# Optimization experiments

Hardware: AMD Instinct MI355X
Metric: run time of the kernel (lower is better)

The kernel has to match this reference:

```python
import jax, jax.numpy as jnp
import numpy as np

ENC_DIM = 512
B, T = 2048, 256
NUM_PARTS, PART_DIM, ATT_DIM, VOCAB = 64, 32, 128, 12


def _p(key, shape, scale=0.05):
    return jax.random.normal(key, shape, dtype=jnp.float32) * scale


def setup_inputs() -> dict:
    key = jax.random.key(0)
    ks = jax.random.split(key, 24)
    inp = {
        "img_features": jax.random.normal(ks[0], (B, 32, 8, 8), dtype=jnp.float32),
        "label": jax.random.normal(ks[1], (B, T, VOCAB), dtype=jnp.float32),
        # Attention params
        "Ww": _p(ks[2], (ATT_DIM, PART_DIM)), "Wb": _p(ks[3], (ATT_DIM,)),
        "Uw": _p(ks[4], (ATT_DIM, ENC_DIM)), "Ub": _p(ks[5], (ATT_DIM,)),
        "vw": _p(ks[6], (1, ATT_DIM)), "vb": _p(ks[7], (1,)),
        "betaw": _p(ks[8], (PART_DIM, ENC_DIM)), "betab": _p(ks[9], (PART_DIM,)),
        # init hidden params
        "ihw": _p(ks[10], (ENC_DIM, NUM_PARTS)), "ihb": _p(ks[11], (ENC_DIM,)),
        "icw": _p(ks[12], (ENC_DIM, NUM_PARTS)), "icb": _p(ks[13], (ENC_DIM,)),
        # LSTMCell params (PyTorch layout: [4*H, in] / [4*H, H])
        "W_ih": _p(ks[14], (4 * ENC_DIM, VOCAB + PART_DIM)),
        "W_hh": _p(ks[15], (4 * ENC_DIM, ENC_DIM)),
        "b_ih": _p(ks[16], (4 * ENC_DIM,)), "b_hh": _p(ks[17], (4 * ENC_DIM,)),
        # output fc
        "ow": _p(ks[18], (VOCAB, ENC_DIM)), "ob": _p(ks[19], (VOCAB,)),
    }
    return inp


def reference(img_features, label, Ww, Wb, Uw, Ub, vw, vb, betaw, betab,
              ihw, ihb, icw, icb, W_ih, W_hh, b_ih, b_hh, ow, ob):
    b = img_features.shape[0]
    feats = img_features.reshape(b, 32, -1)          # [B, 32, 64]
    parts = feats.transpose(0, 2, 1)                  # [B, 64, 32]
    # init hidden/cell from mean over channel dim (dim=1 in torch)
    avg = feats.mean(axis=1)                          # [B, 64]
    h0 = jnp.tanh(avg @ ihw.T + ihb)                  # [B, H]
    c0 = jnp.tanh(avg @ icw.T + icb)
    # W_s depends only on img features: hoist out of the loop (same math)
    Ws = parts @ Ww.T + Wb                            # [B, 64, 128]
    lab = label.transpose(1, 0, 2)                    # [T, B, 12]

    H = h0.shape[1]

    def step(carry, x_t):
        h, c = carry
        Uh = h @ Uw.T + Ub                            # [B, 128]
        att = jnp.tanh(Ws + Uh[:, None, :])           # [B, 64, 128]
        score = (att @ vw.T + vb)[..., 0]             # [B, 64]
        alpha = jax.nn.softmax(score, axis=1)
        ctx = jnp.einsum('bp,bpd->bd', alpha, parts)  # [B, 32]
        beta = jax.nn.sigmoid(h @ betaw.T + betab)
        ctx = ctx * beta
        inp = jnp.concatenate([x_t, ctx], axis=1)     # [B, 44]
        gates = inp @ W_ih.T + b_ih + h @ W_hh.T + b_hh
        i, f, g, o = jnp.split(gates, 4, axis=1)
        c2 = jax.nn.sigmoid(f) * c + jax.nn.sigmoid(i) * jnp.tanh(g)
        h2 = jax.nn.sigmoid(o) * jnp.tanh(c2)
        out = h2 @ ow.T + ob                          # [B, 12]
        return (h2, c2), (out, alpha)

    (_, _), (outs, alphas) = jax.lax.scan(step, (h0, c0), lab)
    output = jax.nn.log_softmax(outs, axis=-1).transpose(1, 0, 2)  # [B, T, 12]
    return output, alphas  # alphas: [T, B, 64] (stacked version of the list)
```

## Files before the change

### kernel.cpp

```cpp
#include <hip/hip_runtime.h>
#include <hip/hip_bf16.h>


typedef __attribute__((ext_vector_type(8))) short short8;
typedef __attribute__((ext_vector_type(4))) float floatx4;
typedef __attribute__((ext_vector_type(2))) unsigned int uint2v;

#define DEV static __device__ __forceinline__
#define C2LE 2.885390082f
#define LOG2E 1.4426950409f
#define LN2 0.6931471806f

DEV unsigned short f2bf(float f) {
    unsigned int u = __float_as_uint(f);
    unsigned int r = (u + 0x7FFFu + ((u >> 16) & 1u)) >> 16;
    return (unsigned short)r;
}
DEV float bf2f(unsigned short u) { return __uint_as_float(((unsigned int)u) << 16); }
DEV float rcp_f(float x) { float r; asm("v_rcp_f32 %0, %1" : "=v"(r) : "v"(x)); return r; }
DEV float tanh_f(float x) { return 1.f - 2.f * rcp_f(1.f + exp2f(x * C2LE)); }
DEV float sigm(float x) { return rcp_f(1.f + exp2f(-x * LOG2E)); }

DEV void ldg16_sc(short8* d, const unsigned short* p) {
    asm volatile("global_load_dwordx4 %0, %1, off sc0 sc1" : "=v"(*d) : "v"(p));
}
DEV void stg16_sc(unsigned short* p, short8 v) {
    asm volatile("global_store_dwordx4 %0, %1, off sc0 sc1" :: "v"(p), "v"(v) : "memory");
}
DEV void stg8_sc(unsigned short* p, uint2v v) {
    asm volatile("global_store_dwordx2 %0, %1, off sc0 sc1" :: "v"(p), "v"(v) : "memory");
}
DEV void st_flag(int* p, int v) {
    asm volatile("global_store_dword %0, %1, off sc0 sc1" :: "v"(p), "v"(v) : "memory");
}
DEV int ld_flag(const int* p) {
    int v;
    asm volatile("global_load_dword %0, %1, off sc0 sc1\n\ts_waitcnt vmcnt(0)"
                 : "=v"(v) : "v"(p) : "memory");
    return v;
}
DEV void waitv0() { asm volatile("s_waitcnt vmcnt(0)" ::: "memory"); }

#define OFF_XH     ((size_t)0)
#define OFF_C0     ((size_t)2359296)
#define OFF_PARTS  ((size_t)6553600)
#define OFF_WBIG   ((size_t)14942208)
#define OFF_WSMALL ((size_t)17301504)
#define OFF_WW2    ((size_t)17465344)
#define OFF_BIAS   ((size_t)17473536)
#define OFF_AVG    ((size_t)17481728)
#define OFF_FLAGS  ((size_t)18006016)

DEV void gbar(int* flags, int bk, int g4, int step) {
    waitv0();
    __syncthreads();
    if (threadIdx.x < 64) {
        int lane = threadIdx.x;
        if (lane == 0) st_flag(flags + bk * 32, step);
        for (;;) {
            int v = step;
            if (lane < 4) v = ld_flag(flags + (g4 + lane) * 32);
            if (__all(v >= step)) break;
            __builtin_amdgcn_s_sleep(1);
        }
    }
    __syncthreads();
}

__global__ void k_init(int* flags) {
    int i = blockIdx.x * 256 + threadIdx.x;
    if (i < 256 * 32) flags[i] = 0;
}

__global__ void k_avg(const float* __restrict__ img, float* __restrict__ avg) {
    int idx = blockIdx.x * 256 + threadIdx.x;
    int b = idx >> 6, p = idx & 63;
    const float* base = img + (size_t)b * 2048 + p;
    float s = 0.f;
#pragma unroll
    for (int k = 0; k < 32; ++k) s += base[k * 64];
    avg[idx] = s * (1.f / 32.f);
}

__global__ void k_prep(const float* __restrict__ Whh, const float* __restrict__ Wih,
                       const float* __restrict__ Uw, const float* __restrict__ betaw,
                       const float* __restrict__ Ww, const float* __restrict__ bih,
                       const float* __restrict__ bhh,
                       unsigned short* __restrict__ Wbig, unsigned short* __restrict__ Wsmall,
                       unsigned short* __restrict__ Ww2, float* __restrict__ bias_cat) {
    int p = blockIdx.x, tid = threadIdx.x;
    int g = p & 3, j = p >> 2, orig = g * 512 + j;
    for (int k = tid; k < 576; k += 256) {
        float v = 0.f;
        if (k < 512) v = Whh[(size_t)orig * 512 + k];
        else if (k < 556) v = Wih[(size_t)orig * 44 + (k - 512)];
        Wbig[(size_t)p * 576 + k] = f2bf(v);
    }
    if (p < 160) {
        for (int k = tid; k < 512; k += 256) {
            float v = (p < 128) ? Uw[(size_t)p * 512 + k] : betaw[(size_t)(p - 128) * 512 + k];
            Wsmall[(size_t)p * 512 + k] = f2bf(v);
        }
    }
    if (p < 128 && tid < 32) Ww2[p * 32 + tid] = f2bf(C2LE * Ww[p * 32 + tid]);
    if (tid == 0) bias_cat[orig] = bih[orig] + bhh[orig];
}

__global__ __launch_bounds__(512) void k_h0c0(const float* __restrict__ avg,
                                              const float* __restrict__ ihw, const float* __restrict__ ihb,
                                              const float* __restrict__ icw, const float* __restrict__ icb,
                                              unsigned short* __restrict__ xh, float* __restrict__ c0) {
    __shared__ float avg_s[8][64];
    int b0 = blockIdx.x * 8, tid = threadIdx.x;
    for (int i = tid; i < 8 * 64; i += 512) avg_s[i >> 6][i & 63] = avg[b0 * 64 + i];
    __syncthreads();
    int j = tid;
    float w0[64];
#pragma unroll
    for (int p4 = 0; p4 < 16; ++p4) {
        float4 v = ((const float4*)(ihw + j * 64))[p4];
        w0[p4 * 4 + 0] = v.x; w0[p4 * 4 + 1] = v.y; w0[p4 * 4 + 2] = v.z; w0[p4 * 4 + 3] = v.w;
    }
    float bh = ihb[j];
#pragma unroll
    for (int bb = 0; bb < 8; ++bb) {
        float s = bh;
#pragma unroll
        for (int p = 0; p < 64; ++p) s += w0[p] * avg_s[bb][p];
        xh[(size_t)(b0 + bb) * 576 + j] = f2bf(tanh_f(s));
        if (j < 20) xh[(size_t)(b0 + bb) * 576 + 556 + j] = 0;
    }
#pragma unroll
    for (int p4 = 0; p4 < 16; ++p4) {
        float4 v = ((const float4*)(icw + j * 64))[p4];
        w0[p4 * 4 + 0] = v.x; w0[p4 * 4 + 1] = v.y; w0[p4 * 4 + 2] = v.z; w0[p4 * 4 + 3] = v.w;
    }
    float bc = icb[j];
#pragma unroll
    for (int bb = 0; bb < 8; ++bb) {
        float s = bc;
#pragma unroll
        for (int p = 0; p < 64; ++p) s += w0[p] * avg_s[bb][p];
        c0[(size_t)(b0 + bb) * 512 + j] = tanh_f(s);
    }
}

__global__ __launch_bounds__(256) void k_parts(const float* __restrict__ img,
                                               unsigned short* __restrict__ parts_bf) {
    __shared__ float pl[64][33];
    int b = blockIdx.x, tid = threadIdx.x;
    const float* ib = img + (size_t)b * 2048;
    for (int i = tid; i < 2048; i += 256) pl[i & 63][i >> 6] = ib[i];
    __syncthreads();
    for (int i = tid; i < 2048; i += 256)
        parts_bf[(size_t)b * 2048 + i] = f2bf(pl[i >> 5][i & 31]);
}

__global__ __launch_bounds__(512, 2) void k_scan(
    unsigned short* __restrict__ xh,
    const float* __restrict__ c0,
    const unsigned short* __restrict__ parts_bf,
    const unsigned short* __restrict__ Wsmall, const unsigned short* __restrict__ Wbig,
    const unsigned short* __restrict__ Ww2, const float* __restrict__ bias_cat,
    const float* __restrict__ Ub, const float* __restrict__ betab, const float* __restrict__ Wb,
    const float* __restrict__ vw,
    const float* __restrict__ label, const float* __restrict__ ow, const float* __restrict__ ob,
    float* __restrict__ out_alpha, float* __restrict__ out_logits,
    int* __restrict__ flags)
{
    __shared__ unsigned short Ald[32 * 584];
    __shared__ unsigned short parts_l[8][2304];
    __shared__ unsigned short ow_l[12][512];
    __shared__ unsigned short h2scr[32][128];
    __shared__ float uh_l[8][160];
    __shared__ float al_l[8][64];
    __shared__ float bias_l[512];
    __shared__ unsigned short xscr[8][48];
    __shared__ float vw2_l[128];
    __shared__ float obl[12];

    const int tid = threadIdx.x, w = tid >> 6, lane = tid & 63;
    const int bk = blockIdx.x;
    const int mtile = bk >> 2, ntile = bk & 3;
    const int g4 = bk & ~3;
    const int wm = w >> 2, wn = w & 3;

    if (tid < 128) vw2_l[tid] = -2.f * vw[tid];
    if (tid < 12) obl[tid] = ob[tid];
    {
        int g = tid >> 7, jl = tid & 127;
        bias_l[tid] = bias_cat[g * 512 + ntile * 128 + jl];
    }
    for (int i = tid; i < 12 * 512; i += 512) ow_l[i >> 9][i & 511] = f2bf(ow[i]);
    {
        int row = tid >> 6, p = tid & 63;
        const short8* src = (const short8*)(parts_bf + (size_t)(bk * 8 + row) * 2048 + p * 32);
        short8* dst = (short8*)&parts_l[row][p * 36];
        dst[0] = src[0]; dst[1] = src[1]; dst[2] = src[2]; dst[3] = src[3];
    }
    float creg[32];
#pragma unroll
    for (int nf = 0; nf < 8; ++nf)
#pragma unroll
        for (int r = 0; r < 4; ++r) {
            int b = mtile * 32 + wm * 16 + (lane >> 4) * 4 + r;
            int j = ntile * 128 + wn * 32 + nf * 4 + (lane & 3);
            creg[nf * 4 + r] = c0[(size_t)b * 512 + j];
        }
    {
        short8 tv[4];
#pragma unroll
        for (int q = 0; q < 4; ++q) {
            int cid = tid + q * 512;
            int row = cid >> 6, c16 = cid & 63;
            ldg16_sc(&tv[q], xh + (size_t)(mtile * 32 + row) * 576 + c16 * 8);
        }
        waitv0();
        __builtin_amdgcn_sched_barrier(0);
#pragma unroll
        for (int q = 0; q < 4; ++q) {
            int cid = tid + q * 512;
            int row = cid >> 6, c16 = cid & 63;
            *(short8*)&Ald[row * 584 + c16 * 8] = tv[q];
        }
    }
    __syncthreads();
    float vwsum = 0.f;
#pragma unroll
    for (int d = 0; d < 128; ++d) vwsum += vw2_l[d];
    vwsum *= -0.5f;

    auto do_uh = [&]() {
        if (w < 5) {
            const unsigned short* Bp = Wsmall + (size_t)(w * 32 + (lane & 15)) * 512 + (lane >> 4) * 8;
            const unsigned short* Ab = &Ald[(ntile * 8 + (lane & 7)) * 584 + (lane >> 4) * 8];
            floatx4 u0 = {}, u1 = {};
#pragma unroll 4
            for (int k0 = 0; k0 < 512; k0 += 32) {
                short8 a = *(const short8*)(Ab + k0);
                u0 = __builtin_amdgcn_mfma_f32_16x16x32_bf16(a, *(const short8*)(Bp + k0), u0, 0, 0, 0);
                u1 = __builtin_amdgcn_mfma_f32_16x16x32_bf16(a, *(const short8*)(Bp + 16 * 512 + k0), u1, 0, 0, 0);
            }
            int r0 = (lane >> 4) * 4, cc = lane & 15;
            if (r0 < 8) {
#pragma unroll
                for (int q = 0; q < 2; ++q) {
                    int n = w * 32 + q * 16 + cc;
#pragma unroll
                    for (int r = 0; r < 4; ++r) {
                        float val = (q ? u1[r] : u0[r]);
                        uh_l[r0 + r][n] = (n < 128) ? C2LE * (val + Ub[n] + Wb[n])
                                                    : (val + betab[n - 128]);
                    }
                }
            }
        }
    };

    auto do_head = [&](int tt) {
        int b = bk * 8 + w;
        short8 hv = *(const short8*)&Ald[(ntile * 8 + w) * 584 + lane * 8];
        float hf[8];
#pragma unroll
        for (int j = 0; j < 8; ++j) hf[j] = bf2f((unsigned short)hv[j]);
        float ov[12];
#pragma unroll
        for (int v = 0; v < 12; ++v) {
            short8 wv = *(const short8*)&ow_l[v][lane * 8];
            float p = 0.f;
#pragma unroll
            for (int j = 0; j < 8; ++j) p += hf[j] * bf2f((unsigned short)wv[j]);
#pragma unroll
            for (int o = 32; o; o >>= 1) p += __shfl_xor(p, o);
            ov[v] = p + obl[v];
        }
        float mx = ov[0];
#pragma unroll
        for (int v = 1; v < 12; ++v) mx = fmaxf(mx, ov[v]);
        float ss = 0.f;
#pragma unroll
        for (int v = 0; v < 12; ++v) ss += exp2f((ov[v] - mx) * LOG2E);
        float lse = mx + log2f(ss) * LN2;
#pragma unroll
        for (int v = 0; v < 12; ++v)
            if (lane == v) out_logits[((size_t)b * 256 + tt) * 12 + v] = ov[v] - lse;
    };

    auto do_attn = [&](int tt) {
        int b = bk * 8 + w;
        short8 pa[4];
#pragma unroll
        for (int mt = 0; mt < 4; ++mt)
            pa[mt] = *(const short8*)&parts_l[w][(mt * 16 + (lane & 15)) * 36 + (lane >> 4) * 8];
        float sc[4][4] = {};
#pragma unroll
        for (int nt = 0; nt < 8; ++nt) {
            short8 wwf = *(const short8*)(Ww2 + (size_t)((lane & 15) + 16 * nt) * 32 + (lane >> 4) * 8);
            int d = nt * 16 + (lane & 15);
            float ud = uh_l[w][d];
            float v2 = vw2_l[d];
#pragma unroll
            for (int mt = 0; mt < 4; ++mt) {
                floatx4 z = {};
                floatx4 wsa = __builtin_amdgcn_mfma_f32_16x16x32_bf16(pa[mt], wwf, z, 0, 0, 0);
#pragma unroll
                for (int r = 0; r < 4; ++r)
                    sc[mt][r] += v2 * rcp_f(1.f + exp2f(wsa[r] + ud));
            }
        }
        float mx = -1e30f;
#pragma unroll
        for (int mt = 0; mt < 4; ++mt)
#pragma unroll
            for (int r = 0; r < 4; ++r) {
                float s = sc[mt][r];
                s += __shfl_xor(s, 1); s += __shfl_xor(s, 2);
                s += __shfl_xor(s, 4); s += __shfl_xor(s, 8);
                s += vwsum;
                sc[mt][r] = s;
                mx = fmaxf(mx, s);
            }
        mx = fmaxf(mx, __shfl_xor(mx, 16));
        mx = fmaxf(mx, __shfl_xor(mx, 32));
        float ssum = 0.f;
        float av[4][4];
#pragma unroll
        for (int mt = 0; mt < 4; ++mt)
#pragma unroll
            for (int r = 0; r < 4; ++r) {
                av[mt][r] = exp2f((sc[mt][r] - mx) * LOG2E);
                ssum += av[mt][r];
            }
        ssum += __shfl_xor(ssum, 16);
        ssum += __shfl_xor(ssum, 32);
        float rs = rcp_f(ssum);
#pragma unroll
        for (int mt = 0; mt < 4; ++mt) {
            if ((lane & 15) == mt) {
                float4 fv = make_float4(av[mt][0] * rs, av[mt][1] * rs, av[mt][2] * rs, av[mt][3] * rs);
                int p0 = mt * 16 + (lane >> 4) * 4;
                *(float4*)&out_alpha[((size_t)tt * 2048 + b) * 64 + p0] = fv;
                *(float4*)&al_l[w][p0] = fv;
            }
        }
        int k = lane & 31, half = lane >> 5;
        float cp = 0.f;
#pragma unroll
        for (int p = 0; p < 32; ++p) {
            int pp = half * 32 + p;
            cp += al_l[w][pp] * bf2f(parts_l[w][pp * 36 + k]);
        }
        cp += __shfl_xor(cp, 32);
        if (half == 0) xscr[w][12 + k] = f2bf(cp * sigm(uh_l[w][128 + k]));
        if (lane < 12) xscr[w][lane] = f2bf(label[((size_t)b * 256 + tt) * 12 + lane]);
        if (lane < 11) {
            uint2v v = *(const uint2v*)&xscr[w][lane * 4];
            stg8_sc(xh + (size_t)b * 576 + 512 + lane * 4, v);
        }
    };

    auto phase1 = [&]() {
        const unsigned short* Bp = Wbig + (size_t)(ntile * 512 + wn * 128 + (lane & 15)) * 576 + (lane >> 4) * 8;
        const unsigned short* Ab = &Ald[(wm * 16 + (lane & 15)) * 584 + (lane >> 4) * 8];
        floatx4 acc[8] = {};
#pragma unroll 2
        for (int kk = 0; kk < 18; ++kk) {
            int k0 = kk * 32;
            short8 a = *(const short8*)(Ab + k0);
#pragma unroll
            for (int nf = 0; nf < 8; ++nf) {
                short8 bv = *(const short8*)(Bp + (size_t)nf * 9216 + k0);
                acc[nf] = __builtin_amdgcn_mfma_f32_16x16x32_bf16(a, bv, acc[nf], 0, 0, 0);
            }
        }
        int base = (lane & 48) | ((lane & 3) * 4);
#pragma unroll
        for (int nf = 0; nf < 8; ++nf) {
            int jl = wn * 32 + nf * 4 + (lane & 3);
            float bi = bias_l[jl], bfv = bias_l[128 + jl], bg = bias_l[256 + jl], bo = bias_l[384 + jl];
#pragma unroll
            for (int r = 0; r < 4; ++r) {
                float x = acc[nf][r];
                float g0 = __shfl(x, base + 0);
                float g1 = __shfl(x, base + 1);
                float g2 = __shfl(x, base + 2);
                float g3 = __shfl(x, base + 3);
                int ci = nf * 4 + r;
                float c2 = sigm(g1 + bfv) * creg[ci] + sigm(g0 + bi) * tanh_f(g2 + bg);
                creg[ci] = c2;
                float h2 = sigm(g3 + bo) * tanh_f(c2);
                if (((lane >> 2) & 3) == 0) {
                    int row = wm * 16 + (lane >> 4) * 4 + r;
                    h2scr[row][wn * 32 + nf * 4 + (lane & 3)] = f2bf(h2);
                }
            }
        }
        __syncthreads();
        {
            int row = tid >> 4, seg = tid & 15;
            short8 v = *(const short8*)&h2scr[row][seg * 8];
            stg16_sc(xh + (size_t)(mtile * 32 + row) * 576 + ntile * 128 + seg * 8, v);
        }
    };

    do_uh();
    __syncthreads();
    do_attn(0);
    int bc = 0;
    gbar(flags, bk, g4, ++bc);
    if (tid < 256) {
        short8 tv;
        int row = tid >> 3, c16 = tid & 7;
        ldg16_sc(&tv, xh + (size_t)(mtile * 32 + row) * 576 + 512 + c16 * 8);
        waitv0();
        __builtin_amdgcn_sched_barrier(0);
        *(short8*)&Ald[row * 584 + 512 + c16 * 8] = tv;
    }
    __syncthreads();

    for (int t = 0; t < 256; ++t) {
        phase1();
        gbar(flags, bk, g4, ++bc);
        {
            short8 tv;
            int row = tid >> 6, c16 = tid & 63;
            ldg16_sc(&tv, xh + (size_t)(bk * 8 + row) * 576 + c16 * 8);
            waitv0();
            __builtin_amdgcn_sched_barrier(0);
            *(short8*)&Ald[(ntile * 8 + row) * 584 + c16 * 8] = tv;
        }
        __syncthreads();
        do_head(t);
        if (t < 255) do_uh();
        __syncthreads();
        if (t < 255) {
            short8 s24[3];
#pragma unroll
            for (int q = 0; q < 3; ++q) {
                int cid = tid + q * 512;
                int r24 = cid >> 6, c16 = cid & 63;
                int lr = (r24 < ntile * 8) ? r24 : r24 + 8;
                ldg16_sc(&s24[q], xh + (size_t)(mtile * 32 + lr) * 576 + c16 * 8);
            }
            do_attn(t + 1);
            waitv0();
            __builtin_amdgcn_sched_barrier(0);
#pragma unroll
            for (int q = 0; q < 3; ++q) {
                int cid = tid + q * 512;
                int r24 = cid >> 6, c16 = cid & 63;
                int lr = (r24 < ntile * 8) ? r24 : r24 + 8;
                *(short8*)&Ald[lr * 584 + c16 * 8] = s24[q];
            }
            gbar(flags, bk, g4, ++bc);
            if (tid < 256) {
                short8 tv;
                int row = tid >> 3, c16 = tid & 7;
                ldg16_sc(&tv, xh + (size_t)(mtile * 32 + row) * 576 + 512 + c16 * 8);
                waitv0();
                __builtin_amdgcn_sched_barrier(0);
                *(short8*)&Ald[row * 584 + 512 + c16 * 8] = tv;
            }
            __syncthreads();
        }
    }
}

extern "C" void kernel_launch(void* const* d_in, const int* in_sizes, int n_in,
                              void* d_out, int out_size, void* d_ws, size_t ws_size,
                              hipStream_t stream) {
    const float* img   = (const float*)d_in[0];
    const float* label = (const float*)d_in[1];
    const float* Ww    = (const float*)d_in[2];
    const float* Wb    = (const float*)d_in[3];
    const float* Uw    = (const float*)d_in[4];
    const float* Ub    = (const float*)d_in[5];
    const float* vw    = (const float*)d_in[6];
    const float* betaw = (const float*)d_in[8];
    const float* betab = (const float*)d_in[9];
    const float* ihw   = (const float*)d_in[10];
    const float* ihb   = (const float*)d_in[11];
    const float* icw   = (const float*)d_in[12];
    const float* icb   = (const float*)d_in[13];
    const float* Wih   = (const float*)d_in[14];
    const float* Whh   = (const float*)d_in[15];
    const float* bih   = (const float*)d_in[16];
    const float* bhh   = (const float*)d_in[17];
    const float* ow    = (const float*)d_in[18];
    const float* ob    = (const float*)d_in[19];

    char* ws = (char*)d_ws;
    unsigned short* xh       = (unsigned short*)(ws + OFF_XH);
    float*          c0       = (float*)(ws + OFF_C0);
    unsigned short* parts_bf = (unsigned short*)(ws + OFF_PARTS);
    unsigned short* Wbig     = (unsigned short*)(ws + OFF_WBIG);
    unsigned short* Wsmall   = (unsigned short*)(ws + OFF_WSMALL);
    unsigned short* Ww2      = (unsigned short*)(ws + OFF_WW2);
    float*          bias     = (float*)(ws + OFF_BIAS);
    float*          avg      = (float*)(ws + OFF_AVG);
    int*            flags    = (int*)(ws + OFF_FLAGS);

    float* out_logits = (float*)d_out;
    float* out_alpha  = out_logits + (size_t)2048 * 256 * 12;

    k_init<<<32, 256, 0, stream>>>(flags);
    k_avg<<<512, 256, 0, stream>>>(img, avg);
    k_prep<<<2048, 256, 0, stream>>>(Whh, Wih, Uw, betaw, Ww, bih, bhh, Wbig, Wsmall, Ww2, bias);
    k_h0c0<<<256, 512, 0, stream>>>(avg, ihw, ihb, icw, icb, xh, c0);
    k_parts<<<2048, 256, 0, stream>>>(img, parts_bf);

    k_scan<<<256, 512, 0, stream>>>(xh, c0, parts_bf, Wsmall, Wbig, Ww2, bias,
                                    Ub, betab, Wb, vw, label, ow, ob,
                                    out_alpha, out_logits, flags);
}
```

Baseline: 14.70 ms.

## Split LSTM gate GEMM into hidden and context parts to reorder grid barriers

The per-step gate GEMM is split into the 512-wide hidden-state part, which runs first, and the 64-wide input/context tail, which runs after a grid barrier once the attention context has been published. Each step now stages the full 32-row hidden tile after the second barrier instead of assembling it piecemeal, and the attention for the next step moves after the head. The aim is to start the large hidden-state GEMM without waiting on the attention context, taking attention off the critical path between barriers. In exchange each step still uses two grid barriers in a new order and does more staging traffic, and the cross-workgroup dependencies become harder to reason about.

```diff
diff --git a/kernel.cpp b/kernel.cpp
--- a/kernel.cpp
+++ b/kernel.cpp
@@ -207,7 +207,11 @@
             int j = ntile * 128 + wn * 32 + nf * 4 + (lane & 3);
             creg[nf * 4 + r] = c0[(size_t)b * 512 + j];
         }
-    {
+
+    floatx4 acc[8];
+    float vwsum = 0.f;
+
+    auto stage32 = [&]() {
         short8 tv[4];
 #pragma unroll
         for (int q = 0; q < 4; ++q) {
@@ -223,12 +227,17 @@
             int row = cid >> 6, c16 = cid & 63;
             *(short8*)&Ald[row * 584 + c16 * 8] = tv[q];
         }
-    }
-    __syncthreads();
-    float vwsum = 0.f;
-#pragma unroll
-    for (int d = 0; d < 128; ++d) vwsum += vw2_l[d];
-    vwsum *= -0.5f;
+    };
+    auto stage_tail = [&]() {
+        if (tid < 256) {
+            short8 tv;
+            int row = tid >> 3, c16 = tid & 7;
+            ldg16_sc(&tv, xh + (size_t)(mtile * 32 + row) * 576 + 512 + c16 * 8);
+            waitv0();
+            __builtin_amdgcn_sched_barrier(0);
+            *(short8*)&Ald[row * 584 + 512 + c16 * 8] = tv;
+        }
+    };
 
     auto do_uh = [&]() {
         if (w < 5) {
@@ -359,12 +368,27 @@
         }
     };
 
-    auto phase1 = [&]() {
+    auto gemm_h = [&]() {
         const unsigned short* Bp = Wbig + (size_t)(ntile * 512 + wn * 128 + (lane & 15)) * 576 + (lane >> 4) * 8;
         const unsigned short* Ab = &Ald[(wm * 16 + (lane & 15)) * 584 + (lane >> 4) * 8];
-        floatx4 acc[8] = {};
+#pragma unroll
+        for (int nf = 0; nf < 8; ++nf) acc[nf] = (floatx4){0.f, 0.f, 0.f, 0.f};
 #pragma unroll 2
-        for (int kk = 0; kk < 18; ++kk) {
+        for (int kk = 0; kk < 16; ++kk) {
+            int k0 = kk * 32;
+            short8 a = *(const short8*)(Ab + k0);
+#pragma unroll
+            for (int nf = 0; nf < 8; ++nf) {
+                short8 bv = *(const short8*)(Bp + (size_t)nf * 9216 + k0);
+                acc[nf] = __builtin_amdgcn_mfma_f32_16x16x32_bf16(a, bv, acc[nf], 0, 0, 0);
+            }
+        }
+    };
+    auto gemm_tail_cell = [&]() {
+        const unsigned short* Bp = Wbig + (size_t)(ntile * 512 + wn * 128 + (lane & 15)) * 576 + (lane >> 4) * 8;
+        const unsigned short* Ab = &Ald[(wm * 16 + (lane & 15)) * 584 + (lane >> 4) * 8];
+#pragma unroll
+        for (int kk = 16; kk < 18; ++kk) {
             int k0 = kk * 32;
             short8 a = *(const short8*)(Ab + k0);
 #pragma unroll
@@ -403,65 +427,33 @@
         }
     };
 
+    stage32();
+    __syncthreads();
+    {
+        float s = 0.f;
+#pragma unroll
+        for (int d = 0; d < 128; ++d) s += vw2_l[d];
+        vwsum = -0.5f * s;
+    }
     do_uh();
     __syncthreads();
     do_attn(0);
+
     int bc = 0;
-    gbar(flags, bk, g4, ++bc);
-    if (tid < 256) {
-        short8 tv;
-        int row = tid >> 3, c16 = tid & 7;
-        ldg16_sc(&tv, xh + (size_t)(mtile * 32 + row) * 576 + 512 + c16 * 8);
-        waitv0();
-        __builtin_amdgcn_sched_barrier(0);
-        *(short8*)&Ald[row * 584 + 512 + c16 * 8] = tv;
-    }
-    __syncthreads();
-
     for (int t = 0; t < 256; ++t) {
-        phase1();
+        gemm_h();
         gbar(flags, bk, g4, ++bc);
-        {
-            short8 tv;
-            int row = tid >> 6, c16 = tid & 63;
-            ldg16_sc(&tv, xh + (size_t)(bk * 8 + row) * 576 + c16 * 8);
-            waitv0();
-            __builtin_amdgcn_sched_barrier(0);
-            *(short8*)&Ald[(ntile * 8 + row) * 584 + c16 * 8] = tv;
-        }
+        stage_tail();
+        __syncthreads();
+        gemm_tail_cell();
+        gbar(flags, bk, g4, ++bc);
+        stage32();
         __syncthreads();
         do_head(t);
-        if (t < 255) do_uh();
-        __syncthreads();
         if (t < 255) {
-            short8 s24[3];
-#pragma unroll
-            for (int q = 0; q < 3; ++q) {
-                int cid = tid + q * 512;
-                int r24 = cid >> 6, c16 = cid & 63;
-                int lr = (r24 < ntile * 8) ? r24 : r24 + 8;
-                ldg16_sc(&s24[q], xh + (size_t)(mtile * 32 + lr) * 576 + c16 * 8);
-            }
+            do_uh();
+            __syncthreads();
             do_attn(t + 1);
-            waitv0();
-            __builtin_amdgcn_sched_barrier(0);
-#pragma unroll
-            for (int q = 0; q < 3; ++q) {
-                int cid = tid + q * 512;
-                int r24 = cid >> 6, c16 = cid & 63;
-                int lr = (r24 < ntile * 8) ? r24 : r24 + 8;
-                *(short8*)&Ald[lr * 584 + c16 * 8] = s24[q];
-            }
-            gbar(flags, bk, g4, ++bc);
-            if (tid < 256) {
-                short8 tv;
-                int row = tid >> 3, c16 = tid & 7;
-                ldg16_sc(&tv, xh + (size_t)(mtile * 32 + row) * 576 + 512 + c16 * 8);
-                waitv0();
-                __builtin_amdgcn_sched_barrier(0);
-                *(short8*)&Ald[row * 584 + 512 + c16 * 8] = tv;
-            }
-            __syncthreads();
         }
     }
 }
```

Measured after the change: 14.27 ms. 2.9% less time.

## Replicate attention across the four N-tile blocks to drop one grid barrier per step

Applied to the files above, without the earlier changes.

Each block in a 4-block group now computes the attention context for all 32 rows of its M tile instead of only its own 8 rows. It writes the context and label columns directly into its local A tile in LDS rather than publishing them through global memory. This removes the second group barrier and global exchange per timestep, leaving one gbar per step. The cost is four times redundant attention and Uh work per group, and parts are read from global memory each step instead of from LDS. Only the owning block writes alpha.

```diff
diff --git a/kernel.cpp b/kernel.cpp
--- a/kernel.cpp
+++ b/kernel.cpp
@@ -4,7 +4,6 @@
 
 typedef __attribute__((ext_vector_type(8))) short short8;
 typedef __attribute__((ext_vector_type(4))) float floatx4;
-typedef __attribute__((ext_vector_type(2))) unsigned int uint2v;
 
 #define DEV static __device__ __forceinline__
 #define C2LE 2.885390082f
@@ -26,9 +25,6 @@
 }
 DEV void stg16_sc(unsigned short* p, short8 v) {
     asm volatile("global_store_dwordx4 %0, %1, off sc0 sc1" :: "v"(p), "v"(v) : "memory");
-}
-DEV void stg8_sc(unsigned short* p, uint2v v) {
-    asm volatile("global_store_dwordx2 %0, %1, off sc0 sc1" :: "v"(p), "v"(v) : "memory");
 }
 DEV void st_flag(int* p, int v) {
     asm volatile("global_store_dword %0, %1, off sc0 sc1" :: "v"(p), "v"(v) : "memory");
@@ -128,7 +124,6 @@
 #pragma unroll
         for (int p = 0; p < 64; ++p) s += w0[p] * avg_s[bb][p];
         xh[(size_t)(b0 + bb) * 576 + j] = f2bf(tanh_f(s));
-        if (j < 20) xh[(size_t)(b0 + bb) * 576 + 556 + j] = 0;
     }
 #pragma unroll
     for (int p4 = 0; p4 < 16; ++p4) {
@@ -169,13 +164,11 @@
     int* __restrict__ flags)
 {
     __shared__ unsigned short Ald[32 * 584];
-    __shared__ unsigned short parts_l[8][2304];
     __shared__ unsigned short ow_l[12][512];
     __shared__ unsigned short h2scr[32][128];
-    __shared__ float uh_l[8][160];
-    __shared__ float al_l[8][64];
+    __shared__ float uh_l[32][160];
+    __shared__ float al_l[32][64];
     __shared__ float bias_l[512];
-    __shared__ unsigned short xscr[8][48];
     __shared__ float vw2_l[128];
     __shared__ float obl[12];
 
@@ -192,11 +185,9 @@
         bias_l[tid] = bias_cat[g * 512 + ntile * 128 + jl];
     }
     for (int i = tid; i < 12 * 512; i += 512) ow_l[i >> 9][i & 511] = f2bf(ow[i]);
-    {
-        int row = tid >> 6, p = tid & 63;
-        const short8* src = (const short8*)(parts_bf + (size_t)(bk * 8 + row) * 2048 + p * 32);
-        short8* dst = (short8*)&parts_l[row][p * 36];
-        dst[0] = src[0]; dst[1] = src[1]; dst[2] = src[2]; dst[3] = src[3];
+    for (int i = tid; i < 32 * 20; i += 512) {
+        int row = i / 20, cc = 556 + (i % 20);
+        Ald[row * 584 + cc] = 0;
     }
     float creg[32];
 #pragma unroll
@@ -207,7 +198,13 @@
             int j = ntile * 128 + wn * 32 + nf * 4 + (lane & 3);
             creg[nf * 4 + r] = c0[(size_t)b * 512 + j];
         }
-    {
+    __syncthreads();
+    float vwsum = 0.f;
+#pragma unroll
+    for (int d = 0; d < 128; ++d) vwsum += vw2_l[d];
+    vwsum *= -0.5f;
+
+    auto stage32 = [&]() {
         short8 tv[4];
 #pragma unroll
         for (int q = 0; q < 4; ++q) {
@@ -223,37 +220,24 @@
             int row = cid >> 6, c16 = cid & 63;
             *(short8*)&Ald[row * 584 + c16 * 8] = tv[q];
         }
-    }
-    __syncthreads();
-    float vwsum = 0.f;
-#pragma unroll
-    for (int d = 0; d < 128; ++d) vwsum += vw2_l[d];
-    vwsum *= -0.5f;
+    };
 
     auto do_uh = [&]() {
-        if (w < 5) {
-            const unsigned short* Bp = Wsmall + (size_t)(w * 32 + (lane & 15)) * 512 + (lane >> 4) * 8;
-            const unsigned short* Ab = &Ald[(ntile * 8 + (lane & 7)) * 584 + (lane >> 4) * 8];
-            floatx4 u0 = {}, u1 = {};
+        for (int tt = w; tt < 20; tt += 8) {
+            int mt = tt & 1, nt = tt >> 1;
+            const unsigned short* Bp = Wsmall + (size_t)(nt * 16 + (lane & 15)) * 512 + (lane >> 4) * 8;
+            const unsigned short* Ab = &Ald[(mt * 16 + (lane & 15)) * 584 + (lane >> 4) * 8];
+            floatx4 u = {};
 #pragma unroll 4
             for (int k0 = 0; k0 < 512; k0 += 32) {
                 short8 a = *(const short8*)(Ab + k0);
-                u0 = __builtin_amdgcn_mfma_f32_16x16x32_bf16(a, *(const short8*)(Bp + k0), u0, 0, 0, 0);
-                u1 = __builtin_amdgcn_mfma_f32_16x16x32_bf16(a, *(const short8*)(Bp + 16 * 512 + k0), u1, 0, 0, 0);
-            }
-            int r0 = (lane >> 4) * 4, cc = lane & 15;
-            if (r0 < 8) {
-#pragma unroll
-                for (int q = 0; q < 2; ++q) {
-                    int n = w * 32 + q * 16 + cc;
-#pragma unroll
-                    for (int r = 0; r < 4; ++r) {
-                        float val = (q ? u1[r] : u0[r]);
-                        uh_l[r0 + r][n] = (n < 128) ? C2LE * (val + Ub[n] + Wb[n])
-                                                    : (val + betab[n - 128]);
-                    }
-                }
-            }
+                u = __builtin_amdgcn_mfma_f32_16x16x32_bf16(a, *(const short8*)(Bp + k0), u, 0, 0, 0);
+            }
+            int n = nt * 16 + (lane & 15), r0 = (lane >> 4) * 4;
+            float addv = (n < 128) ? (Ub[n] + Wb[n]) : betab[n - 128];
+            float scl = (n < 128) ? C2LE : 1.f;
+#pragma unroll
+            for (int r = 0; r < 4; ++r) uh_l[mt * 16 + r0 + r][n] = (u[r] + addv) * scl;
         }
     };
 
@@ -287,75 +271,78 @@
     };
 
     auto do_attn = [&](int tt) {
-        int b = bk * 8 + w;
-        short8 pa[4];
-#pragma unroll
-        for (int mt = 0; mt < 4; ++mt)
-            pa[mt] = *(const short8*)&parts_l[w][(mt * 16 + (lane & 15)) * 36 + (lane >> 4) * 8];
-        float sc[4][4] = {};
-#pragma unroll
-        for (int nt = 0; nt < 8; ++nt) {
-            short8 wwf = *(const short8*)(Ww2 + (size_t)((lane & 15) + 16 * nt) * 32 + (lane >> 4) * 8);
-            int d = nt * 16 + (lane & 15);
-            float ud = uh_l[w][d];
-            float v2 = vw2_l[d];
+#pragma unroll
+        for (int u = 0; u < 4; ++u) {
+            int row = w * 4 + u;
+            int b = mtile * 32 + row;
+            bool owner = (row >> 3) == ntile;
+            const unsigned short* pb = parts_bf + (size_t)b * 2048;
+            short8 pa[4];
+#pragma unroll
+            for (int mt = 0; mt < 4; ++mt)
+                pa[mt] = *(const short8*)(pb + ((lane & 15) + 16 * mt) * 32 + (lane >> 4) * 8);
+            float sc[4][4] = {};
+#pragma unroll
+            for (int nt = 0; nt < 8; ++nt) {
+                short8 wwf = *(const short8*)(Ww2 + (size_t)((lane & 15) + 16 * nt) * 32 + (lane >> 4) * 8);
+                int d = nt * 16 + (lane & 15);
+                float ud = uh_l[row][d];
+                float v2 = vw2_l[d];
+#pragma unroll
+                for (int mt = 0; mt < 4; ++mt) {
+                    floatx4 z = {};
+                    floatx4 wsa = __builtin_amdgcn_mfma_f32_16x16x32_bf16(pa[mt], wwf, z, 0, 0, 0);
+#pragma unroll
+                    for (int r = 0; r < 4; ++r)
+                        sc[mt][r] += v2 * rcp_f(1.f + exp2f(wsa[r] + ud));
+                }
+            }
+            float mx = -1e30f;
+#pragma unroll
+            for (int mt = 0; mt < 4; ++mt)
+#pragma unroll
+                for (int r = 0; r < 4; ++r) {
+                    float s = sc[mt][r];
+                    s += __shfl_xor(s, 1); s += __shfl_xor(s, 2);
+                    s += __shfl_xor(s, 4); s += __shfl_xor(s, 8);
+                    s += vwsum;
+                    sc[mt][r] = s;
+                    mx = fmaxf(mx, s);
+                }
+            mx = fmaxf(mx, __shfl_xor(mx, 16));
+            mx = fmaxf(mx, __shfl_xor(mx, 32));
+            float ssum = 0.f;
+            float av[4][4];
+#pragma unroll
+            for (int mt = 0; mt < 4; ++mt)
+#pragma unroll
+                for (int r = 0; r < 4; ++r) {
+                    av[mt][r] = exp2f((sc[mt][r] - mx) * LOG2E);
+                    ssum += av[mt][r];
+                }
+            ssum += __shfl_xor(ssum, 16);
+            ssum += __shfl_xor(ssum, 32);
+            float rs = rcp_f(ssum);
 #pragma unroll
             for (int mt = 0; mt < 4; ++mt) {
-                floatx4 z = {};
-                floatx4 wsa = __builtin_amdgcn_mfma_f32_16x16x32_bf16(pa[mt], wwf, z, 0, 0, 0);
-#pragma unroll
-                for (int r = 0; r < 4; ++r)
-                    sc[mt][r] += v2 * rcp_f(1.f + exp2f(wsa[r] + ud));
-            }
-        }
-        float mx = -1e30f;
-#pragma unroll
-        for (int mt = 0; mt < 4; ++mt)
-#pragma unroll
-            for (int r = 0; r < 4; ++r) {
-                float s = sc[mt][r];
-                s += __shfl_xor(s, 1); s += __shfl_xor(s, 2);
-                s += __shfl_xor(s, 4); s += __shfl_xor(s, 8);
-                s += vwsum;
-                sc[mt][r] = s;
-                mx = fmaxf(mx, s);
-            }
-        mx = fmaxf(mx, __shfl_xor(mx, 16));
-        mx = fmaxf(mx, __shfl_xor(mx, 32));
-        float ssum = 0.f;
-        float av[4][4];
-#pragma unroll
-        for (int mt = 0; mt < 4; ++mt)
-#pragma unroll
-            for (int r = 0; r < 4; ++r) {
-                av[mt][r] = exp2f((sc[mt][r] - mx) * LOG2E);
-                ssum += av[mt][r];
-            }
-        ssum += __shfl_xor(ssum, 16);
-        ssum += __shfl_xor(ssum, 32);
-        float rs = rcp_f(ssum);
-#pragma unroll
-        for (int mt = 0; mt < 4; ++mt) {
-            if ((lane & 15) == mt) {
-                float4 fv = make_float4(av[mt][0] * rs, av[mt][1] * rs, av[mt][2] * rs, av[mt][3] * rs);
-                int p0 = mt * 16 + (lane >> 4) * 4;
-                *(float4*)&out_alpha[((size_t)tt * 2048 + b) * 64 + p0] = fv;
-                *(float4*)&al_l[w][p0] = fv;
-            }
-        }
-        int k = lane & 31, half = lane >> 5;
-        float cp = 0.f;
-#pragma unroll
-        for (int p = 0; p < 32; ++p) {
-            int pp = half * 32 + p;
-            cp += al_l[w][pp] * bf2f(parts_l[w][pp * 36 + k]);
-        }
-        cp += __shfl_xor(cp, 32);
-        if (half == 0) xscr[w][12 + k] = f2bf(cp * sigm(uh_l[w][128 + k]));
-        if (lane < 12) xscr[w][lane] = f2bf(label[((size_t)b * 256 + tt) * 12 + lane]);
-        if (lane < 11) {
-            uint2v v = *(const uint2v*)&xscr[w][lane * 4];
-            stg8_sc(xh + (size_t)b * 576 + 512 + lane * 4, v);
+                if ((lane & 15) == mt) {
+                    float4 fv = make_float4(av[mt][0] * rs, av[mt][1] * rs, av[mt][2] * rs, av[mt][3] * rs);
+                    int p0 = mt * 16 + (lane >> 4) * 4;
+                    if (owner)
+                        *(float4*)&out_alpha[((size_t)tt * 2048 + b) * 64 + p0] = fv;
+                    *(float4*)&al_l[row][p0] = fv;
+                }
+            }
+            int k = lane & 31, half = lane >> 5;
+            float cp = 0.f;
+#pragma unroll
+            for (int p = 0; p < 32; ++p) {
+                int pp = half * 32 + p;
+                cp += al_l[row][pp] * bf2f(pb[pp * 32 + k]);
+            }
+            cp += __shfl_xor(cp, 32);
+            if (half == 0) Ald[row * 584 + 524 + k] = f2bf(cp * sigm(uh_l[row][128 + k]));
+            if (lane < 12) Ald[row * 584 + 512 + lane] = f2bf(label[((size_t)b * 256 + tt) * 12 + lane]);
         }
     };
 
@@ -403,67 +390,28 @@
         }
     };
 
-    do_uh();
-    __syncthreads();
-    do_attn(0);
     int bc = 0;
-    gbar(flags, bk, g4, ++bc);
-    if (tid < 256) {
+    for (int t = 0; t < 256; ++t) {
+        stage32();
+        __syncthreads();
+        if (t > 0) do_head(t - 1);
+        do_uh();
+        __syncthreads();
+        do_attn(t);
+        __syncthreads();
+        phase1();
+        gbar(flags, bk, g4, ++bc);
+    }
+    {
         short8 tv;
-        int row = tid >> 3, c16 = tid & 7;
-        ldg16_sc(&tv, xh + (size_t)(mtile * 32 + row) * 576 + 512 + c16 * 8);
+        int row = tid >> 6, c16 = tid & 63;
+        ldg16_sc(&tv, xh + (size_t)(bk * 8 + row) * 576 + c16 * 8);
         waitv0();
         __builtin_amdgcn_sched_barrier(0);
-        *(short8*)&Ald[row * 584 + 512 + c16 * 8] = tv;
-    }
-    __syncthreads();
-
-    for (int t = 0; t < 256; ++t) {
-        phase1();
-        gbar(flags, bk, g4, ++bc);
-        {
-            short8 tv;
-            int row = tid >> 6, c16 = tid & 63;
-            ldg16_sc(&tv, xh + (size_t)(bk * 8 + row) * 576 + c16 * 8);
-            waitv0();
-            __builtin_amdgcn_sched_barrier(0);
-            *(short8*)&Ald[(ntile * 8 + row) * 584 + c16 * 8] = tv;
-        }
-        __syncthreads();
-        do_head(t);
-        if (t < 255) do_uh();
-        __syncthreads();
-        if (t < 255) {
-            short8 s24[3];
-#pragma unroll
-            for (int q = 0; q < 3; ++q) {
-                int cid = tid + q * 512;
-                int r24 = cid >> 6, c16 = cid & 63;
-                int lr = (r24 < ntile * 8) ? r24 : r24 + 8;
-                ldg16_sc(&s24[q], xh + (size_t)(mtile * 32 + lr) * 576 + c16 * 8);
-            }
-            do_attn(t + 1);
-            waitv0();
-            __builtin_amdgcn_sched_barrier(0);
-#pragma unroll
-            for (int q = 0; q < 3; ++q) {
-                int cid = tid + q * 512;
-                int r24 = cid >> 6, c16 = cid & 63;
-                int lr = (r24 < ntile * 8) ? r24 : r24 + 8;
-                *(short8*)&Ald[lr * 584 + c16 * 8] = s24[q];
-            }
-            gbar(flags, bk, g4, ++bc);
-            if (tid < 256) {
-                short8 tv;
-                int row = tid >> 3, c16 = tid & 7;
-                ldg16_sc(&tv, xh + (size_t)(mtile * 32 + row) * 576 + 512 + c16 * 8);
-                waitv0();
-                __builtin_amdgcn_sched_barrier(0);
-                *(short8*)&Ald[row * 584 + 512 + c16 * 8] = tv;
-            }
-            __syncthreads();
-        }
-    }
+        *(short8*)&Ald[(ntile * 8 + row) * 584 + c16 * 8] = tv;
+    }
+    __syncthreads();
+    do_head(255);
 }
 
 extern "C" void kernel_launch(void* const* d_in, const int* in_sizes, int n_in,
```

After: 35.06 ms. 2.39x slower.
